# Kernel optimization log

Hardware: AMD Instinct MI355X
Metric: run time of the kernel (lower is better)

## Reference

```python
import jax, jax.numpy as jnp
import numpy as np

D_MODEL = 1024
NUM_HEADS = 16
D_K = D_MODEL // NUM_HEADS
THETA = 10000.0
BATCH, SEQ = 2, 2048


def apply_rope(x, token_positions, theta):
    # x: [..., heads, seq, d_k]; interleaved pair rotation
    d = x.shape[-1]
    inv_freq = theta ** (-jnp.arange(0, d, 2, dtype=jnp.float32) / d)  # [d/2]
    ang = token_positions.astype(jnp.float32)[:, None] * inv_freq[None, :]  # [seq, d/2]
    cos, sin = jnp.cos(ang), jnp.sin(ang)  # broadcast over batch/heads
    x_even = x[..., 0::2]
    x_odd = x[..., 1::2]
    out_even = x_even * cos - x_odd * sin
    out_odd = x_even * sin + x_odd * cos
    out = jnp.stack([out_even, out_odd], axis=-1)  # [..., seq, d/2, 2]
    return out.reshape(x.shape)


def setup_inputs() -> dict:
    key = jax.random.key(0)
    ks = jax.random.split(key, 5)
    scale = 1.0 / np.sqrt(D_MODEL)
    return {
        "x": jax.random.normal(ks[0], (BATCH, SEQ, D_MODEL), dtype=jnp.float32),
        "wq": jax.random.normal(ks[1], (D_MODEL, D_MODEL), dtype=jnp.float32) * scale,
        "wk": jax.random.normal(ks[2], (D_MODEL, D_MODEL), dtype=jnp.float32) * scale,
        "wv": jax.random.normal(ks[3], (D_MODEL, D_MODEL), dtype=jnp.float32) * scale,
        "wo": jax.random.normal(ks[4], (D_MODEL, D_MODEL), dtype=jnp.float32) * scale,
        "token_positions": jnp.arange(SEQ, dtype=jnp.int32),
    }


def reference(x, wq, wk, wv, wo, token_positions):
    B, S, _ = x.shape
    # fused-style QKV projections: weight layout is [d_out, d_in]
    xq = jnp.einsum("bsd,kd->bsk", x, wq)
    xk = jnp.einsum("bsd,kd->bsk", x, wk)
    xv = jnp.einsum("bsd,vd->bsv", x, wv)
    # split heads: [b, h, s, d_h]
    def split(t):
        return t.reshape(B, S, NUM_HEADS, D_K).transpose(0, 2, 1, 3)
    xq, xk, xv = split(xq), split(xk), split(xv)
    xq = apply_rope(xq, token_positions, THETA)
    xk = apply_rope(xk, token_positions, THETA)
    scores = jnp.einsum("bhqd,bhkd->bhqk", xq, xk) / jnp.sqrt(jnp.float32(D_K))
    causal = jnp.tril(jnp.ones((S, S), dtype=bool))
    scores = jnp.where(causal, scores, -jnp.inf)
    attn = jax.nn.softmax(scores, axis=-1)
    out = jnp.einsum("bhqk,bhkd->bhqd", attn, xv)
    out = out.transpose(0, 2, 1, 3).reshape(B, S, D_MODEL)  # merge heads
    return jnp.einsum("bsv,dv->bsd", out, wo)
```

## Files before the change

### kernel.cpp

```cpp
#include <hip/hip_runtime.h>

typedef __attribute__((ext_vector_type(8))) short short8;
typedef __attribute__((ext_vector_type(4))) short short4v;
typedef __attribute__((ext_vector_type(4))) float floatx4;

__device__ inline ushort f2b(float f) {
    union { uint i; float f; } c; c.f = f;
    uint i = c.i;
    uint r = (i + 0x7FFFu + ((i >> 16) & 1u)) >> 16;
    return (ushort)r;
}

__device__ __forceinline__ void load_lds16(const ushort* g, ushort* l) {
    __builtin_amdgcn_global_load_lds((const __attribute__((address_space(1))) void*)g,
                                     (__attribute__((address_space(3))) void*)l, 16, 0, 0);
}

__global__ __launch_bounds__(256) void cvt4_k(const float* __restrict__ x,
                                              const float* __restrict__ wq,
                                              const float* __restrict__ wk,
                                              const float* __restrict__ wv,
                                              ushort* __restrict__ xb,
                                              ushort* __restrict__ wqb,
                                              ushort* __restrict__ wkb,
                                              ushort* __restrict__ wvb,
                                              const int* __restrict__ pos,
                                              float2* __restrict__ tab) {
    const int blk = blockIdx.x;
    if (blk >= 3584) {
        const int idx = (blk - 3584) * 256 + threadIdx.x;
        const int s = idx >> 5, fi = idx & 31;
        const float inv = exp2f(-(float)fi * 0.41524101186092557f);
        const float ang = (float)pos[s] * inv;
        float sn, cs;
        sincosf(ang, &sn, &cs);
        tab[idx] = make_float2(cs, sn);
        return;
    }
    const float* in; ushort* out; int base;
    if (blk < 2048)      { in = x;  out = xb;  base = blk; }
    else if (blk < 2560) { in = wq; out = wqb; base = blk - 2048; }
    else if (blk < 3072) { in = wk; out = wkb; base = blk - 2560; }
    else                 { in = wv; out = wvb; base = blk - 3072; }
    const int i = (base * 256 + threadIdx.x) * 8;
    float4 f0 = *(const float4*)(in + i);
    float4 f1 = *(const float4*)(in + i + 4);
    ushort u[8] = {f2b(f0.x), f2b(f0.y), f2b(f0.z), f2b(f0.w),
                   f2b(f1.x), f2b(f1.y), f2b(f1.z), f2b(f1.w)};
    *(uint4*)(out + i) = *(const uint4*)u;
}

__global__ __launch_bounds__(256) void cvt_k(const float* __restrict__ in,
                                             ushort* __restrict__ out, int n) {
    const int i = (blockIdx.x * 256 + threadIdx.x) * 8;
    if (i >= n) return;
    float4 f0 = *(const float4*)(in + i);
    float4 f1 = *(const float4*)(in + i + 4);
    ushort u[8] = {f2b(f0.x), f2b(f0.y), f2b(f0.z), f2b(f0.w),
                   f2b(f1.x), f2b(f1.y), f2b(f1.z), f2b(f1.w)};
    *(uint4*)(out + i) = *(const uint4*)u;
}

template <bool OUTF32>
__device__ __forceinline__ void gemm_body(ushort* As, ushort* Bs,
                                          const ushort* __restrict__ A,
                                          const ushort* __restrict__ B,
                                          void* __restrict__ C,
                                          int N, int m0, int n0,
                                          bool doRope, const float2* __restrict__ tab,
                                          float oscale) {
    const int tid = threadIdx.x;
    const int wave = tid >> 6, lane = tid & 63;
    const int quad = lane >> 4, l16 = lane & 15;
    const int wm = (wave >> 1) * 64, wn = (wave & 1) * 64;

    floatx4 acc[4][4] = {};

    const int cA = tid, cB = tid + 256;
    const int rA = cA >> 2, jgA = ((cA & 3) - (rA >> 1)) & 3;
    const int rB = cB >> 2, jgB = ((cB & 3) - (rB >> 1)) & 3;
    const ushort* gaA = A + (size_t)(m0 + rA) * 1024 + jgA * 8;
    const ushort* gaB = A + (size_t)(m0 + rB) * 1024 + jgB * 8;
    const ushort* gbA = B + (size_t)(n0 + rA) * 1024 + jgA * 8;
    const ushort* gbB = B + (size_t)(n0 + rB) * 1024 + jgB * 8;

    load_lds16(gaA, As + cA * 8);
    load_lds16(gaB, As + cB * 8);
    load_lds16(gbA, Bs + cA * 8);
    load_lds16(gbB, Bs + cB * 8);
    __syncthreads();

    for (int kt = 0; kt < 32; ++kt) {
        const int cur = kt & 1;
        if (kt + 1 < 32) {
            const int nb = (cur ^ 1) * 4096;
            load_lds16(gaA + (kt + 1) * 32, As + nb + cA * 8);
            load_lds16(gaB + (kt + 1) * 32, As + nb + cB * 8);
            load_lds16(gbA + (kt + 1) * 32, Bs + nb + cA * 8);
            load_lds16(gbB + (kt + 1) * 32, Bs + nb + cB * 8);
        }
        const ushort* as = As + cur * 4096;
        const ushort* bs = Bs + cur * 4096;
        short8 af[4], bf[4];
#pragma unroll
        for (int i = 0; i < 4; ++i) {
            const int ra = wm + i * 16 + l16;
            const int rb = wn + i * 16 + l16;
            af[i] = *(const short8*)(as + ra * 32 + (((quad + (ra >> 1)) & 3) << 3));
            bf[i] = *(const short8*)(bs + rb * 32 + (((quad + (rb >> 1)) & 3) << 3));
        }
#pragma unroll
        for (int mi = 0; mi < 4; ++mi)
#pragma unroll
            for (int ni = 0; ni < 4; ++ni)
                acc[mi][ni] = __builtin_amdgcn_mfma_f32_16x16x32_bf16(af[mi], bf[ni], acc[mi][ni], 0, 0, 0);
        __syncthreads();
    }
#pragma unroll
    for (int mi = 0; mi < 4; ++mi) {
        const int row = m0 + wm + mi * 16 + quad * 4;
#pragma unroll
        for (int ni = 0; ni < 4; ++ni) {
            const int col = n0 + wn + ni * 16 + l16;
            const int fi = ((wn + ni * 16 + l16) & 63) >> 1;
#pragma unroll
            for (int r = 0; r < 4; ++r) {
                float v = acc[mi][ni][r];
                if (doRope) {
                    const float other = __shfl_xor(v, 1);
                    const float2 cs = tab[((row + r) & 2047) * 32 + fi];
                    v = (col & 1) ? (other * cs.y + v * cs.x) : (v * cs.x - other * cs.y);
                }
                v *= oscale;
                if (OUTF32) ((float*)C)[(size_t)(row + r) * N + col] = v;
                else        ((ushort*)C)[(size_t)(row + r) * N + col] = f2b(v);
            }
        }
    }
}

__global__ __launch_bounds__(256) void gemm_qkv(const ushort* __restrict__ xb,
                                                const ushort* __restrict__ wqb,
                                                const ushort* __restrict__ wkb,
                                                const ushort* __restrict__ wvb,
                                                ushort* __restrict__ q,
                                                ushort* __restrict__ k,
                                                ushort* __restrict__ vt,
                                                const float2* __restrict__ tab) {
    __shared__ __align__(16) ushort As[8192], Bs[8192];
    const int blk = blockIdx.x;
    const int job = blk >> 8, r = blk & 255;
    const ushort *A, *B;
    ushort* C;
    int N, m0, n0;
    bool rope;
    float osc;
    if (job == 0)      { A = xb;  B = wqb; C = q;  N = 1024; m0 = (r >> 3) * 128; n0 = (r & 7) * 128; rope = true;  osc = 0.18033688011112042f; }
    else if (job == 1) { A = xb;  B = wkb; C = k;  N = 1024; m0 = (r >> 3) * 128; n0 = (r & 7) * 128; rope = true;  osc = 1.0f; }
    else               { A = wvb; B = xb;  C = vt; N = 4096; m0 = (r & 7) * 128;  n0 = (r >> 3) * 128; rope = false; osc = 1.0f; }
    gemm_body<false>(As, Bs, A, B, C, N, m0, n0, rope, tab, osc);
}

__global__ __launch_bounds__(256) void gemm_o(const ushort* __restrict__ A,
                                              const ushort* __restrict__ B,
                                              float* __restrict__ C) {
    __shared__ __align__(16) ushort As[8192], Bs[8192];
    gemm_body<true>(As, Bs, A, B, C, 1024, blockIdx.y * 128, blockIdx.x * 128, false, nullptr, 1.0f);
}

__global__ __launch_bounds__(256, 4) void attn_k(const ushort* __restrict__ Qg,
                                                 const ushort* __restrict__ Kg,
                                                 const ushort* __restrict__ Vtg,
                                                 ushort* __restrict__ Og) {
    __shared__ __align__(16) ushort Ks[2][4096];
    __shared__ __align__(16) ushort Vs[2][4096];

    const int tid = threadIdx.x;
    const int wave = tid >> 6, lane = tid & 63;
    const int quad = lane >> 4, l16 = lane & 15;
    const int blk = blockIdx.x;
    const int bh = blk & 31;
    const int qt = 31 - (blk >> 5);
    const int b = bh >> 4, h = bh & 15;
    const int bq = b * 2048;
    const int wl = wave * 16 + l16;
    const int nk = qt + 1, dt = nk - 1;

    const int cA = tid, cB = tid + 256;
    const int sA = cA >> 3, jA = ((cA & 7) - sA) & 7;
    const int sB = cB >> 3, jB = ((cB & 7) - sB) & 7;
    const ushort* kgA = Kg + (size_t)(bq + sA) * 1024 + h * 64 + jA * 8;
    const ushort* kgB = Kg + (size_t)(bq + sB) * 1024 + h * 64 + jB * 8;
    const ushort* vgA = Vtg + (size_t)(h * 64 + sA) * 4096 + bq + jA * 8;
    const ushort* vgB = Vtg + (size_t)(h * 64 + sB) * 4096 + bq + jB * 8;

    const int kb0 = l16 * 64 + (((quad + l16) & 7) << 3);
    const int kb1 = l16 * 64 + (((quad + 4 + l16) & 7) << 3);
    int vbs[4];
#pragma unroll
    for (int cb = 0; cb < 4; ++cb)
        vbs[cb] = l16 * 64 + (((cb * 2 + (quad >> 1) + l16) & 7) << 3) + (quad & 1) * 4;

    const ushort* qrow = Qg + (size_t)(bq + qt * 64 + wl) * 1024 + h * 64 + quad * 8;
    const short8 qf0 = *(const short8*)qrow;
    const short8 qf1 = *(const short8*)(qrow + 32);

    floatx4 od[4] = {};
    float l_st = 0.0f;

    load_lds16(kgA, &Ks[0][cA * 8]);
    load_lds16(kgB, &Ks[0][cB * 8]);
    load_lds16(vgA, &Vs[0][cA * 8]);
    load_lds16(vgB, &Vs[0][cB * 8]);
    __syncthreads();

    const ushort* kgA2 = kgA + 65536;
    const ushort* kgB2 = kgB + 65536;
    const ushort* vgA2 = vgA + 64;
    const ushort* vgB2 = vgB + 64;

    for (int kt = 0; kt < nk; ++kt) {
        const int cur = kt & 1;
        if (kt + 1 < nk) {
            const int nxt = cur ^ 1;
            load_lds16(kgA2, &Ks[nxt][cA * 8]);
            load_lds16(kgB2, &Ks[nxt][cB * 8]);
            load_lds16(vgA2, &Vs[nxt][cA * 8]);
            load_lds16(vgB2, &Vs[nxt][cB * 8]);
            kgA2 += 65536; kgB2 += 65536; vgA2 += 64; vgB2 += 64;
        }
        const ushort* kc = &Ks[cur][0];
        const ushort* vc = &Vs[cur][0];

        floatx4 st[4];
        __builtin_amdgcn_s_setprio(1);
#pragma unroll
        for (int cb = 0; cb < 4; ++cb) {
            short8 kf0 = *(const short8*)(kc + kb0 + cb * 1024);
            short8 kf1 = *(const short8*)(kc + kb1 + cb * 1024);
            floatx4 z = {};
            z = __builtin_amdgcn_mfma_f32_16x16x32_bf16(kf0, qf0, z, 0, 0, 0);
            z = __builtin_amdgcn_mfma_f32_16x16x32_bf16(kf1, qf1, z, 0, 0, 0);
            st[cb] = z;
        }
        __builtin_amdgcn_s_setprio(0);

        const bool diag = (kt == dt);
        float pv[4][4];
        float sum = 0.0f;
#pragma unroll
        for (int cb = 0; cb < 4; ++cb) {
            const int scb = cb * 16 + quad * 4;
#pragma unroll
            for (int r = 0; r < 4; ++r) {
                float e = exp2f(st[cb][r]);
                if (diag && (scb + r > wl)) e = 0.0f;
                pv[cb][r] = e;
                sum += e;
            }
        }
        sum += __shfl_xor(sum, 16);
        sum += __shfl_xor(sum, 32);
        l_st += sum;

        short4v pb[4];
#pragma unroll
        for (int cb = 0; cb < 4; ++cb) {
            uint lo_, hi_;
            asm("v_cvt_pk_bf16_f32 %0, %1, %2" : "=v"(lo_) : "v"(pv[cb][0]), "v"(pv[cb][1]));
            asm("v_cvt_pk_bf16_f32 %0, %1, %2" : "=v"(hi_) : "v"(pv[cb][2]), "v"(pv[cb][3]));
            union { uint u[2]; short4v s; } cvu;
            cvu.u[0] = lo_; cvu.u[1] = hi_;
            pb[cb] = cvu.s;
        }

        __builtin_amdgcn_s_setprio(1);
#pragma unroll
        for (int db = 0; db < 4; ++db) {
#pragma unroll
            for (int cb = 0; cb < 4; ++cb) {
                short4v vf = *(const short4v*)(vc + vbs[cb] + db * 1024);
                od[db] = __builtin_amdgcn_mfma_f32_16x16x16bf16_1k(vf, pb[cb], od[db], 0, 0, 0);
            }
        }
        __builtin_amdgcn_s_setprio(0);
        __syncthreads();
    }

    const float linv = 1.0f / l_st;
    ushort* orow = Og + (size_t)(bq + qt * 64 + wl) * 1024 + h * 64 + quad * 4;
#pragma unroll
    for (int db = 0; db < 4; ++db) {
        uint2 w;
        w.x = (uint)f2b(od[db][0] * linv) | ((uint)f2b(od[db][1] * linv) << 16);
        w.y = (uint)f2b(od[db][2] * linv) | ((uint)f2b(od[db][3] * linv) << 16);
        *(uint2*)(orow + db * 16) = w;
    }
}

extern "C" void kernel_launch(void* const* d_in, const int* in_sizes, int n_in,
                              void* d_out, int out_size, void* d_ws, size_t ws_size,
                              hipStream_t stream) {
    const float* x  = (const float*)d_in[0];
    const float* wq = (const float*)d_in[1];
    const float* wk = (const float*)d_in[2];
    const float* wv = (const float*)d_in[3];
    const float* wo = (const float*)d_in[4];
    const int* pos  = (const int*)d_in[5];

    const size_t NX = (size_t)4096 * 1024;
    const size_t NW = (size_t)1024 * 1024;

    ushort* q_ws  = (ushort*)d_ws;
    ushort* k_ws  = q_ws + NX;
    ushort* vt_ws = k_ws + NX;
    ushort* o_ws  = vt_ws + NX;
    ushort* xb  = (ushort*)d_out;
    ushort* wqb = xb + NX;
    ushort* wkb = wqb + NW;
    ushort* wvb = wkb + NW;
    float2* tab = (float2*)(wvb + NW);

    cvt4_k<<<dim3(3840), 256, 0, stream>>>(x, wq, wk, wv, xb, wqb, wkb, wvb, pos, tab);
    gemm_qkv<<<dim3(768), 256, 0, stream>>>(xb, wqb, wkb, wvb, q_ws, k_ws, vt_ws, tab);
    attn_k<<<dim3(1024), 256, 0, stream>>>(q_ws, k_ws, vt_ws, o_ws);
    cvt_k<<<dim3(512), 256, 0, stream>>>(wo, q_ws, (int)NW);
    gemm_o<<<dim3(8, 32), 256, 0, stream>>>(o_ws, q_ws, (float*)d_out);
}
```

Before: 201.2 us.

## Fuse wo conversion into output GEMM, swizzle block order, peel diagonal attention tile

Removes the separate fp32-to-bf16 conversion kernel for wo. The output GEMM now loads fp32 wo tiles into registers, converts them, and writes them into LDS after the MFMAs, which saves one launch and one round trip through global memory. It also remaps block indices in the QKV and output GEMMs so consecutive blocks share operand tiles for better L2 reuse. The attention loop is split into non-diagonal steps plus a peeled final diagonal step that skips the prefetch and the trailing barrier. In exchange, the B operand of the output GEMM is read at twice the bytes and its register pressure goes up.

```diff
diff --git a/kernel.cpp b/kernel.cpp
--- a/kernel.cpp
+++ b/kernel.cpp
@@ -50,21 +50,11 @@
     *(uint4*)(out + i) = *(const uint4*)u;
 }
 
-__global__ __launch_bounds__(256) void cvt_k(const float* __restrict__ in,
-                                             ushort* __restrict__ out, int n) {
-    const int i = (blockIdx.x * 256 + threadIdx.x) * 8;
-    if (i >= n) return;
-    float4 f0 = *(const float4*)(in + i);
-    float4 f1 = *(const float4*)(in + i + 4);
-    ushort u[8] = {f2b(f0.x), f2b(f0.y), f2b(f0.z), f2b(f0.w),
-                   f2b(f1.x), f2b(f1.y), f2b(f1.z), f2b(f1.w)};
-    *(uint4*)(out + i) = *(const uint4*)u;
-}
-
-template <bool OUTF32>
+template <bool OUTF32, bool BF32>
 __device__ __forceinline__ void gemm_body(ushort* As, ushort* Bs,
                                           const ushort* __restrict__ A,
-                                          const ushort* __restrict__ B,
+                                          const ushort* __restrict__ Bb,
+                                          const float* __restrict__ B32,
                                           void* __restrict__ C,
                                           int N, int m0, int n0,
                                           bool doRope, const float2* __restrict__ tab,
@@ -81,23 +71,51 @@
     const int rB = cB >> 2, jgB = ((cB & 3) - (rB >> 1)) & 3;
     const ushort* gaA = A + (size_t)(m0 + rA) * 1024 + jgA * 8;
     const ushort* gaB = A + (size_t)(m0 + rB) * 1024 + jgB * 8;
-    const ushort* gbA = B + (size_t)(n0 + rA) * 1024 + jgA * 8;
-    const ushort* gbB = B + (size_t)(n0 + rB) * 1024 + jgB * 8;
+    const ushort* gbA = nullptr;
+    const ushort* gbB = nullptr;
+    const float*  hbA = nullptr;
+    const float*  hbB = nullptr;
+    if constexpr (!BF32) {
+        gbA = Bb + (size_t)(n0 + rA) * 1024 + jgA * 8;
+        gbB = Bb + (size_t)(n0 + rB) * 1024 + jgB * 8;
+    } else {
+        hbA = B32 + (size_t)(n0 + rA) * 1024 + jgA * 8;
+        hbB = B32 + (size_t)(n0 + rB) * 1024 + jgB * 8;
+    }
 
     load_lds16(gaA, As + cA * 8);
     load_lds16(gaB, As + cB * 8);
-    load_lds16(gbA, Bs + cA * 8);
-    load_lds16(gbB, Bs + cB * 8);
+    if constexpr (!BF32) {
+        load_lds16(gbA, Bs + cA * 8);
+        load_lds16(gbB, Bs + cB * 8);
+    } else {
+        float4 a0 = *(const float4*)hbA, a1 = *(const float4*)(hbA + 4);
+        float4 b0 = *(const float4*)hbB, b1 = *(const float4*)(hbB + 4);
+        ushort ua[8] = {f2b(a0.x), f2b(a0.y), f2b(a0.z), f2b(a0.w),
+                        f2b(a1.x), f2b(a1.y), f2b(a1.z), f2b(a1.w)};
+        ushort ub[8] = {f2b(b0.x), f2b(b0.y), f2b(b0.z), f2b(b0.w),
+                        f2b(b1.x), f2b(b1.y), f2b(b1.z), f2b(b1.w)};
+        *(uint4*)(Bs + cA * 8) = *(const uint4*)ua;
+        *(uint4*)(Bs + cB * 8) = *(const uint4*)ub;
+    }
     __syncthreads();
 
     for (int kt = 0; kt < 32; ++kt) {
         const int cur = kt & 1;
+        const int nb = (cur ^ 1) * 4096;
+        float4 pa0, pa1, pb0, pb1;
         if (kt + 1 < 32) {
-            const int nb = (cur ^ 1) * 4096;
             load_lds16(gaA + (kt + 1) * 32, As + nb + cA * 8);
             load_lds16(gaB + (kt + 1) * 32, As + nb + cB * 8);
-            load_lds16(gbA + (kt + 1) * 32, Bs + nb + cA * 8);
-            load_lds16(gbB + (kt + 1) * 32, Bs + nb + cB * 8);
+            if constexpr (!BF32) {
+                load_lds16(gbA + (kt + 1) * 32, Bs + nb + cA * 8);
+                load_lds16(gbB + (kt + 1) * 32, Bs + nb + cB * 8);
+            } else {
+                const float* pA = hbA + (kt + 1) * 32;
+                const float* pB = hbB + (kt + 1) * 32;
+                pa0 = *(const float4*)pA; pa1 = *(const float4*)(pA + 4);
+                pb0 = *(const float4*)pB; pb1 = *(const float4*)(pB + 4);
+            }
         }
         const ushort* as = As + cur * 4096;
         const ushort* bs = Bs + cur * 4096;
@@ -114,6 +132,16 @@
 #pragma unroll
             for (int ni = 0; ni < 4; ++ni)
                 acc[mi][ni] = __builtin_amdgcn_mfma_f32_16x16x32_bf16(af[mi], bf[ni], acc[mi][ni], 0, 0, 0);
+        if constexpr (BF32) {
+            if (kt + 1 < 32) {
+                ushort ua[8] = {f2b(pa0.x), f2b(pa0.y), f2b(pa0.z), f2b(pa0.w),
+                                f2b(pa1.x), f2b(pa1.y), f2b(pa1.z), f2b(pa1.w)};
+                ushort ub[8] = {f2b(pb0.x), f2b(pb0.y), f2b(pb0.z), f2b(pb0.w),
+                                f2b(pb1.x), f2b(pb1.y), f2b(pb1.z), f2b(pb1.w)};
+                *(uint4*)(Bs + nb + cA * 8) = *(const uint4*)ua;
+                *(uint4*)(Bs + nb + cB * 8) = *(const uint4*)ub;
+            }
+        }
         __syncthreads();
     }
 #pragma unroll
@@ -149,7 +177,8 @@
                                                 const float2* __restrict__ tab) {
     __shared__ __align__(16) ushort As[8192], Bs[8192];
     const int blk = blockIdx.x;
-    const int job = blk >> 8, r = blk & 255;
+    const int swz = (blk & 7) * 96 + (blk >> 3);
+    const int job = swz >> 8, r = swz & 255;
     const ushort *A, *B;
     ushort* C;
     int N, m0, n0;
@@ -158,14 +187,17 @@
     if (job == 0)      { A = xb;  B = wqb; C = q;  N = 1024; m0 = (r >> 3) * 128; n0 = (r & 7) * 128; rope = true;  osc = 0.18033688011112042f; }
     else if (job == 1) { A = xb;  B = wkb; C = k;  N = 1024; m0 = (r >> 3) * 128; n0 = (r & 7) * 128; rope = true;  osc = 1.0f; }
     else               { A = wvb; B = xb;  C = vt; N = 4096; m0 = (r & 7) * 128;  n0 = (r >> 3) * 128; rope = false; osc = 1.0f; }
-    gemm_body<false>(As, Bs, A, B, C, N, m0, n0, rope, tab, osc);
+    gemm_body<false, false>(As, Bs, A, B, nullptr, C, N, m0, n0, rope, tab, osc);
 }
 
 __global__ __launch_bounds__(256) void gemm_o(const ushort* __restrict__ A,
-                                              const ushort* __restrict__ B,
+                                              const float* __restrict__ wo,
                                               float* __restrict__ C) {
     __shared__ __align__(16) ushort As[8192], Bs[8192];
-    gemm_body<true>(As, Bs, A, B, C, 1024, blockIdx.y * 128, blockIdx.x * 128, false, nullptr, 1.0f);
+    const int blk = blockIdx.x;
+    const int swz = (blk & 7) * 32 + (blk >> 3);
+    const int m = swz >> 3, n = swz & 7;
+    gemm_body<true, true>(As, Bs, A, nullptr, wo, C, 1024, m * 128, n * 128, false, nullptr, 1.0f);
 }
 
 __global__ __launch_bounds__(256, 4) void attn_k(const ushort* __restrict__ Qg,
@@ -219,9 +251,9 @@
     const ushort* vgA2 = vgA + 64;
     const ushort* vgB2 = vgB + 64;
 
-    for (int kt = 0; kt < nk; ++kt) {
+    auto step = [&](int kt, bool diag, bool pref) {
         const int cur = kt & 1;
-        if (kt + 1 < nk) {
+        if (pref) {
             const int nxt = cur ^ 1;
             load_lds16(kgA2, &Ks[nxt][cA * 8]);
             load_lds16(kgB2, &Ks[nxt][cB * 8]);
@@ -245,7 +277,6 @@
         }
         __builtin_amdgcn_s_setprio(0);
 
-        const bool diag = (kt == dt);
         float pv[4][4];
         float sum = 0.0f;
 #pragma unroll
@@ -284,8 +315,11 @@
             }
         }
         __builtin_amdgcn_s_setprio(0);
-        __syncthreads();
-    }
+        if (pref) __syncthreads();
+    };
+
+    for (int kt = 0; kt < dt; ++kt) step(kt, false, true);
+    step(dt, true, false);
 
     const float linv = 1.0f / l_st;
     ushort* orow = Og + (size_t)(bq + qt * 64 + wl) * 1024 + h * 64 + quad * 4;
@@ -324,6 +358,5 @@
     cvt4_k<<<dim3(3840), 256, 0, stream>>>(x, wq, wk, wv, xb, wqb, wkb, wvb, pos, tab);
     gemm_qkv<<<dim3(768), 256, 0, stream>>>(xb, wqb, wkb, wvb, q_ws, k_ws, vt_ws, tab);
     attn_k<<<dim3(1024), 256, 0, stream>>>(q_ws, k_ws, vt_ws, o_ws);
-    cvt_k<<<dim3(512), 256, 0, stream>>>(wo, q_ws, (int)NW);
-    gemm_o<<<dim3(8, 32), 256, 0, stream>>>(o_ws, q_ws, (float*)d_out);
-}
+    gemm_o<<<dim3(256), 256, 0, stream>>>(o_ws, wo, (float*)d_out);
+}
```

After: 203.8 us. About the same (+1.3%).
